# Kernel optimization log

Measured on AMD Instinct MI355X. Metric: run time of the kernel, lower is better.

## Reference

```python
import jax, jax.numpy as jnp
import numpy as np

# Model hyperparameters (from init_kwargs)
SIG = 10.0      # kernel length scale 'sig'
C = 0.0         # energy integration constant 'c'
STD = 1.0       # data std 'std'
N_ATOMS = 21    # aspirin-like molecule
T_ROWS = 12000  # n_train * n_perms (permutation-expanded training rows)
DESC = N_ATOMS * (N_ATOMS - 1) // 2  # 210
BATCH = 64


def setup_inputs() -> dict:
    key = jax.random.key(0)
    k1, k2, k3 = jax.random.split(key, 3)
    # Geometries: M x N x 3 Cartesian coordinates (spread out so atoms are distinct)
    Rs = jax.random.normal(k1, (BATCH, N_ATOMS, 3), dtype=jnp.float32) * 2.0
    # Permutation-expanded training descriptors (inverse distances -> positive)
    xs_train = jax.random.uniform(k2, (T_ROWS, DESC), dtype=jnp.float32, minval=0.05, maxval=1.0)
    Jx_alphas = jax.random.normal(k3, (T_ROWS, DESC), dtype=jnp.float32)
    return {"Rs": Rs, "xs_train": xs_train, "Jx_alphas": Jx_alphas}


def reference(Rs, xs_train, Jx_alphas):
    sig = SIG
    q = np.sqrt(5.0) / sig
    M, N, _ = Rs.shape
    i, j = np.tril_indices(N, k=-1)

    # Pairwise atomic displacement vectors and distances. Diagonal is padded with 1
    # (instead of inf as in the torch code) -- every diagonal contribution below is
    # multiplied by an exact zero (expand_tril zeroes the diagonal, diffs diag = 0),
    # so the value is irrelevant but this keeps gradients finite.
    diffs = Rs[:, :, None, :] - Rs[:, None, :, :]          # [M, N, N, 3]
    eye = jnp.eye(N, dtype=Rs.dtype)
    dists = jnp.sqrt(jnp.sum(diffs * diffs, axis=-1) + eye)  # [M, N, N]

    # Inverse-distance descriptor (strict lower triangle)
    xs = 1.0 / dists[:, i, j]                              # [M, DESC]

    # Descriptor-space differences vs all (permuted) training points
    x_diffs = (q * xs)[:, None, :] - q * xs_train[None]    # [M, T, DESC]
    x_dists = jnp.sqrt(jnp.sum(x_diffs * x_diffs, axis=-1))  # [M, T]

    # Matern-5/2 kernel pieces
    exp_xs = (5.0 / (3.0 * sig * sig)) * jnp.exp(-x_dists)   # [M, T]
    dot_x_diff_Jx = jnp.einsum('mtd,td->mt', x_diffs, Jx_alphas)  # [M, T]
    exp_xs_1_x_dists = exp_xs * (1.0 + x_dists)              # [M, T]

    # Descriptor-space force pieces
    F1s_x = jnp.einsum('mt,mtd->md', exp_xs * dot_x_diff_Jx, x_diffs)  # [M, DESC]
    F2s_x = exp_xs_1_x_dists @ Jx_alphas                               # [M, DESC]
    Fs_x = (F1s_x - F2s_x) * STD

    # expand_tril: scatter descriptor-space forces into symmetric NxN with zero diag
    full = jnp.zeros((M, N, N), dtype=Rs.dtype)
    full = full.at[:, i, j].set(Fs_x).at[:, j, i].set(Fs_x)

    # Cartesian forces: sum over first atom index (torch's .sum(dim=1))
    Fs = jnp.einsum('mab,mabk->mbk', full / dists ** 3, diffs)  # [M, N, 3]

    # Energies
    Es = jnp.sum(exp_xs_1_x_dists * dot_x_diff_Jx, axis=-1) / q
    Es = C + Es * STD
    return Es, Fs
```

## Files before the change

kernel.cpp:

```cpp
#include <hip/hip_runtime.h>
#include <hip/hip_fp16.h>
#include <math.h>

#define N_ATOMS 21
#define DESC 210
#define APAD 224
#define T_ROWS 12000
#define BATCH 64
#define NBLK_A 250
#define TROWS_B 48
#define PCW 216

#define QCONST 0.22360679774997896f
#define K0CONST (1.0f/60.0f)

typedef short bf16x8 __attribute__((ext_vector_type(8)));
typedef float f32x4 __attribute__((ext_vector_type(4)));

__device__ __forceinline__ float u2f(unsigned int u) {
    union { unsigned int u; float f; } x; x.u = u; return x.f;
}
__device__ __forceinline__ unsigned short f2bf(float f) {
    union { float f; unsigned int u; } x; x.f = f;
    unsigned int r = x.u + 0x7fffu + ((x.u >> 16) & 1u);
    return (unsigned short)(r >> 16);
}
__device__ __forceinline__ float bf2f(unsigned short h) {
    return u2f((unsigned int)h << 16);
}

__global__ __launch_bounds__(256) void k_prep(const float* __restrict__ Rs,
                                              unsigned short* __restrict__ Abf,
                                              float* __restrict__ na2) {
    int m = blockIdx.x;
    __shared__ float R[N_ATOMS * 3];
    __shared__ float red[256];
    int tid = threadIdx.x;
    if (tid < N_ATOMS * 3) R[tid] = Rs[m * N_ATOMS * 3 + tid];
    __syncthreads();
    float val = 0.f;
    if (tid < DESC) {
        int p = tid;
        int i = (int)((1.0f + sqrtf(1.0f + 8.0f * (float)p)) * 0.5f);
        while (i * (i - 1) / 2 > p) --i;
        while ((i + 1) * i / 2 <= p) ++i;
        int j = p - i * (i - 1) / 2;
        float dx = R[i * 3 + 0] - R[j * 3 + 0];
        float dy = R[i * 3 + 1] - R[j * 3 + 1];
        float dz = R[i * 3 + 2] - R[j * 3 + 2];
        float d = sqrtf(dx * dx + dy * dy + dz * dz);
        val = QCONST / d;
    }
    unsigned short h = f2bf(val);
    if (tid < APAD) Abf[m * APAD + tid] = h;
    float va = bf2f(h);
    red[tid] = va * va;
    __syncthreads();
    for (int s = 128; s > 0; s >>= 1) {
        if (tid < s) red[tid] += red[tid + s];
        __syncthreads();
    }
    if (tid == 0) na2[m] = red[0];
}

#define BS_OFF 0
#define JS_OFF 22272
#define XT_OFF 44544
#define W_OFF  91136
#define NB_OFF 104448
#define BJ_OFF 104640
#define NA_OFF 104832
#define LDS_SZ 105088

__global__ __launch_bounds__(256) void k_fused(const float* __restrict__ Btr,
                                               const float* __restrict__ Jx,
                                               const unsigned short* __restrict__ Abf,
                                               const float* __restrict__ na2,
                                               float* __restrict__ es_p,
                                               float* __restrict__ rs_p,
                                               __half* __restrict__ pC) {
    __shared__ char lds[LDS_SZ];
    const int blk = blockIdx.x;
    const int t0 = blk * TROWS_B;
    const int tid = threadIdx.x;
    const int lane = tid & 63;
    const int w = __builtin_amdgcn_readfirstlane(tid >> 6);
    const int lr = lane & 15;
    const int kb = lane >> 4;

    uint4 au[7];
    {
        const unsigned short* ap = Abf + (w * 16 + lr) * APAD + kb * 8;
#pragma unroll
        for (int k8 = 0; k8 < 7; k8++) au[k8] = *(const uint4*)(ap + k8 * 32);
    }
    if (tid < 64) *(float*)(lds + NA_OFF + tid * 4) = na2[tid];

#pragma unroll
    for (int pass = 0; pass < 2; ++pass) {
        if (pass == 1 && tid >= 128) break;
        const int g = pass * 32 + (tid >> 3);
        const int gl = tid & 7;
        const int tr = t0 + g;
        const float* bp = Btr + (size_t)tr * DESC;
        const float* jp = Jx + (size_t)tr * DESC;
        float nb = 0.f, bj = 0.f;
#pragma unroll
        for (int it = 0; it < 15; it++) {
            int c = it * 8 + gl;
            if (c < 116) {
                float2 vb = make_float2(0.f, 0.f), vj = make_float2(0.f, 0.f);
                if (c < 105) {
                    vb = *(const float2*)(bp + 2 * c);
                    vj = *(const float2*)(jp + 2 * c);
                }
                unsigned short hbx = f2bf(vb.x), hby = f2bf(vb.y);
                unsigned short hjx = f2bf(vj.x), hjy = f2bf(vj.y);
                *(unsigned int*)(lds + BS_OFF + g * 464 + c * 4) = (unsigned)hbx | ((unsigned)hby << 16);
                *(unsigned int*)(lds + JS_OFF + g * 464 + c * 4) = (unsigned)hjx | ((unsigned)hjy << 16);
                if (c < 112) {
                    const int d = 2 * c;
                    *(unsigned short*)(lds + XT_OFF + d * 208 + g * 2) = hbx;
                    *(unsigned short*)(lds + XT_OFF + (d + 1) * 208 + g * 2) = hby;
                    *(unsigned short*)(lds + XT_OFF + d * 208 + 96 + g * 2) = hjx;
                    *(unsigned short*)(lds + XT_OFF + (d + 1) * 208 + 96 + g * 2) = hjy;
                }
                float fbx = bf2f(hbx), fby = bf2f(hby);
                float fjx = bf2f(hjx), fjy = bf2f(hjy);
                nb = fmaf(fbx, fbx, nb); nb = fmaf(fby, fby, nb);
                bj = fmaf(fbx, fjx, bj); bj = fmaf(fby, fjy, bj);
            }
        }
#pragma unroll
        for (int m = 1; m < 8; m <<= 1) { nb += __shfl_xor(nb, m); bj += __shfl_xor(bj, m); }
        if (gl == 0) {
            *(float*)(lds + NB_OFF + g * 4) = nb;
            *(float*)(lds + BJ_OFF + g * 4) = bj;
        }
    }
    __syncthreads();

    f32x4 accP[3] = {{0.f,0.f,0.f,0.f},{0.f,0.f,0.f,0.f},{0.f,0.f,0.f,0.f}};
    f32x4 accQ[3] = {{0.f,0.f,0.f,0.f},{0.f,0.f,0.f,0.f},{0.f,0.f,0.f,0.f}};
#pragma unroll
    for (int k8 = 0; k8 < 7; k8++) {
        union { uint4 u; bf16x8 h; } a;
        a.u = au[k8];
#pragma unroll
        for (int nt = 0; nt < 3; nt++) {
            union { uint4 u; bf16x8 h; } bu, ju;
            const int ro = (nt * 16 + lr) * 464 + k8 * 64 + kb * 16;
            bu.u = *(const uint4*)(lds + BS_OFF + ro);
            ju.u = *(const uint4*)(lds + JS_OFF + ro);
            accP[nt] = __builtin_amdgcn_mfma_f32_16x16x32_bf16(a.h, bu.h, accP[nt], 0, 0, 0);
            accQ[nt] = __builtin_amdgcn_mfma_f32_16x16x32_bf16(a.h, ju.h, accQ[nt], 0, 0, 0);
        }
    }

    float na4[4];
#pragma unroll
    for (int r = 0; r < 4; r++)
        na4[r] = *(const float*)(lds + NA_OFF + (w * 16 + kb * 4 + r) * 4);
    float es4[4] = {0.f,0.f,0.f,0.f}, rs4[4] = {0.f,0.f,0.f,0.f};
#pragma unroll
    for (int nt = 0; nt < 3; nt++) {
        const int row = nt * 16 + lr;
        const float nb_c = *(const float*)(lds + NB_OFF + row * 4);
        const float bj_c = *(const float*)(lds + BJ_OFF + row * 4);
#pragma unroll
        for (int r = 0; r < 4; r++) {
            float S = na4[r] + QCONST * QCONST * nb_c - 2.f * QCONST * accP[nt][r];
            float xd = sqrtf(fmaxf(S, 0.f));
            float e = K0CONST * __expf(-xd);
            float dot = accQ[nt][r] - QCONST * bj_c;
            float w1 = e * dot;
            float w2 = e * (1.f + xd);
            es4[r] += w2 * dot; rs4[r] += w1;
            const int mrow = w * 16 + kb * 4 + r;
            *(unsigned short*)(lds + W_OFF + mrow * 208 + row * 2) = f2bf(QCONST * w1);
            *(unsigned short*)(lds + W_OFF + mrow * 208 + 96 + row * 2) = f2bf(w2);
        }
    }
#pragma unroll
    for (int m = 1; m < 16; m <<= 1) {
#pragma unroll
        for (int r = 0; r < 4; r++) {
            es4[r] += __shfl_xor(es4[r], m);
            rs4[r] += __shfl_xor(rs4[r], m);
        }
    }
    if (lr == 0) {
#pragma unroll
        for (int r = 0; r < 4; r++) {
            es_p[(size_t)(w * 16 + kb * 4 + r) * NBLK_A + blk] = es4[r];
            rs_p[(size_t)(w * 16 + kb * 4 + r) * NBLK_A + blk] = rs4[r];
        }
    }
    __syncthreads();

    {
        union { uint4 u; bf16x8 h; } wa[3];
        const char* Wp = lds + W_OFF + (w * 16 + lr) * 208;
#pragma unroll
        for (int c = 0; c < 3; c++) wa[c].u = *(const uint4*)(Wp + c * 64 + kb * 16);
        __half* D = (__half*)lds;
#pragma unroll
        for (int dt = 0; dt < 14; dt++) {
            const char* Xp = lds + XT_OFF + (dt * 16 + lr) * 208;
            f32x4 acc = {0.f, 0.f, 0.f, 0.f};
#pragma unroll
            for (int c = 0; c < 3; c++) {
                union { uint4 u; bf16x8 h; } xb;
                xb.u = *(const uint4*)(Xp + c * 64 + kb * 16);
                acc = __builtin_amdgcn_mfma_f32_16x16x32_bf16(wa[c].h, xb.h, acc, 0, 0, 0);
            }
#pragma unroll
            for (int r = 0; r < 4; r++)
                D[(w * 16 + kb * 4 + r) * 224 + dt * 16 + lr] = __float2half(acc[r]);
        }
    }
    __syncthreads();

    {
        const char* D = (const char*)lds;
        for (int i = tid; i < 64 * 27; i += 256) {
            const int mrow = i / 27, oct = i % 27;
            uint4 v = *(const uint4*)(D + mrow * 448 + oct * 16);
            *(uint4*)((char*)pC + (((size_t)mrow * NBLK_A + blk) * PCW + oct * 8) * 2) = v;
        }
    }
}

__global__ __launch_bounds__(256) void k_final(const float* __restrict__ Rs,
                                               const unsigned short* __restrict__ Abf,
                                               const float* __restrict__ es_p,
                                               const float* __restrict__ rs_p,
                                               const __half* __restrict__ pC,
                                               float* __restrict__ out) {
    const int m = blockIdx.x;
    const int tid = threadIdx.x;
    __shared__ float parts[27][8][8];
    __shared__ float fsx[DESC];
    __shared__ float R[N_ATOMS * 3];
    __shared__ float s_rs, s_es;
    if (tid < N_ATOMS * 3) R[tid] = Rs[m * N_ATOMS * 3 + tid];
    if (tid < 216) {
        const int cg = tid / 27, o = tid % 27;
        float facc[8];
#pragma unroll
        for (int e = 0; e < 8; e++) facc[e] = 0.f;
        const __half* base = pC + (size_t)m * NBLK_A * PCW + o * 8;
#pragma unroll 4
        for (int c = cg; c < NBLK_A; c += 8) {
            uint4 v = *(const uint4*)(base + (size_t)c * PCW);
            const __half2* h = (const __half2*)&v;
#pragma unroll
            for (int p2 = 0; p2 < 4; p2++) {
                float2 f = __half22float2(h[p2]);
                facc[p2 * 2] += f.x;
                facc[p2 * 2 + 1] += f.y;
            }
        }
#pragma unroll
        for (int e = 0; e < 8; e++) parts[o][cg][e] = facc[e];
    }
    __syncthreads();
    if (tid < 64) {
        float es = 0.f, rs = 0.f;
        for (int c2 = tid; c2 < NBLK_A; c2 += 64) {
            es += es_p[(size_t)m * NBLK_A + c2];
            rs += rs_p[(size_t)m * NBLK_A + c2];
        }
        for (int mask = 1; mask < 64; mask <<= 1) {
            es += __shfl_xor(es, mask);
            rs += __shfl_xor(rs, mask);
        }
        if (tid == 0) { s_es = es; s_rs = rs; }
    }
    __syncthreads();
    if (tid < DESC) {
        float s = 0.f;
        const int o = tid >> 3, e = tid & 7;
#pragma unroll
        for (int cg = 0; cg < 8; cg++) s += parts[o][cg][e];
        fsx[tid] = s_rs * bf2f(Abf[m * APAD + tid]) - s;
    }
    if (tid == 0) out[m] = s_es * (1.0f / QCONST);
    __syncthreads();
    if (tid < N_ATOMS * 3) {
        int b = tid / 3, kk = tid % 3;
        float acc = 0.f;
        for (int a = 0; a < N_ATOMS; a++) {
            if (a == b) continue;
            float dx = R[a * 3 + 0] - R[b * 3 + 0];
            float dy = R[a * 3 + 1] - R[b * 3 + 1];
            float dz = R[a * 3 + 2] - R[b * 3 + 2];
            float d2 = dx * dx + dy * dy + dz * dz;
            float dist = sqrtf(d2);
            float inv3 = 1.0f / (d2 * dist);
            int hi = (a > b) ? a : b, lo = (a > b) ? b : a;
            int p = hi * (hi - 1) / 2 + lo;
            float diffk = (kk == 0) ? dx : ((kk == 1) ? dy : dz);
            acc = fmaf(fsx[p] * inv3, diffk, acc);
        }
        out[BATCH + m * N_ATOMS * 3 + tid] = acc;
    }
}

extern "C" void kernel_launch(void* const* d_in, const int* in_sizes, int n_in,
                              void* d_out, int out_size, void* d_ws, size_t ws_size,
                              hipStream_t stream) {
    (void)in_sizes; (void)n_in; (void)out_size; (void)ws_size;
    const float* Rs = (const float*)d_in[0];
    const float* Btr = (const float*)d_in[1];
    const float* Jx = (const float*)d_in[2];
    float* out = (float*)d_out;

    char* ws = (char*)d_ws;
    unsigned short* Abf = (unsigned short*)ws;  ws += (size_t)BATCH * APAD * 2;
    float* na2 = (float*)ws;                    ws += BATCH * 4;
    float* es_p = (float*)ws;                   ws += (size_t)BATCH * NBLK_A * 4;
    float* rs_p = (float*)ws;                   ws += (size_t)BATCH * NBLK_A * 4;
    __half* pC = (__half*)ws;

    k_prep<<<dim3(BATCH), dim3(256), 0, stream>>>(Rs, Abf, na2);
    k_fused<<<dim3(NBLK_A), dim3(256), 0, stream>>>(Btr, Jx, Abf, na2, es_p, rs_p, pC);
    k_final<<<dim3(BATCH), dim3(256), 0, stream>>>(Rs, Abf, es_p, rs_p, pC, out);
}
```

Before: 33.32 us.

## Fold descriptor prep into fused kernel and widen blocks to 512 threads

Removes the separate prep kernel: every fused block recomputes all 64 inverse-distance descriptors and their norms into LDS, and block 0 writes them out for the final kernel. The fused and final kernels move to 512 threads, splitting the MFMA tiles and the load work across twice as many waves, with per-block partial energy sums reduced in LDS first. This saves one launch and raises occupancy and latency hiding, at the cost of redundant descriptor work in every block and extra barriers.

Result: slower. 39.90 us (+19.8%).

```diff
diff --git a/kernel.cpp b/kernel.cpp
--- a/kernel.cpp
+++ b/kernel.cpp
@@ -7,7 +7,7 @@
 #define APAD 224
 #define T_ROWS 12000
 #define BATCH 64
-#define NBLK_A 250
+#define NBLK 250
 #define TROWS_B 48
 #define PCW 216
 
@@ -27,40 +27,6 @@
 }
 __device__ __forceinline__ float bf2f(unsigned short h) {
     return u2f((unsigned int)h << 16);
-}
-
-__global__ __launch_bounds__(256) void k_prep(const float* __restrict__ Rs,
-                                              unsigned short* __restrict__ Abf,
-                                              float* __restrict__ na2) {
-    int m = blockIdx.x;
-    __shared__ float R[N_ATOMS * 3];
-    __shared__ float red[256];
-    int tid = threadIdx.x;
-    if (tid < N_ATOMS * 3) R[tid] = Rs[m * N_ATOMS * 3 + tid];
-    __syncthreads();
-    float val = 0.f;
-    if (tid < DESC) {
-        int p = tid;
-        int i = (int)((1.0f + sqrtf(1.0f + 8.0f * (float)p)) * 0.5f);
-        while (i * (i - 1) / 2 > p) --i;
-        while ((i + 1) * i / 2 <= p) ++i;
-        int j = p - i * (i - 1) / 2;
-        float dx = R[i * 3 + 0] - R[j * 3 + 0];
-        float dy = R[i * 3 + 1] - R[j * 3 + 1];
-        float dz = R[i * 3 + 2] - R[j * 3 + 2];
-        float d = sqrtf(dx * dx + dy * dy + dz * dz);
-        val = QCONST / d;
-    }
-    unsigned short h = f2bf(val);
-    if (tid < APAD) Abf[m * APAD + tid] = h;
-    float va = bf2f(h);
-    red[tid] = va * va;
-    __syncthreads();
-    for (int s = 128; s > 0; s >>= 1) {
-        if (tid < s) red[tid] += red[tid + s];
-        __syncthreads();
-    }
-    if (tid == 0) na2[m] = red[0];
 }
 
 #define BS_OFF 0
@@ -70,12 +36,13 @@
 #define NB_OFF 104448
 #define BJ_OFF 104640
 #define NA_OFF 104832
-#define LDS_SZ 105088
-
-__global__ __launch_bounds__(256) void k_fused(const float* __restrict__ Btr,
+#define ES_OFF 105088
+#define LDS_SZ 106624
+
+__global__ __launch_bounds__(512) void k_fused(const float* __restrict__ Rs,
+                                               const float* __restrict__ Btr,
                                                const float* __restrict__ Jx,
-                                               const unsigned short* __restrict__ Abf,
-                                               const float* __restrict__ na2,
+                                               unsigned short* __restrict__ Abf,
                                                float* __restrict__ es_p,
                                                float* __restrict__ rs_p,
                                                __half* __restrict__ pC) {
@@ -87,125 +54,203 @@
     const int w = __builtin_amdgcn_readfirstlane(tid >> 6);
     const int lr = lane & 15;
     const int kb = lane >> 4;
-
+    const int mt = w & 3;
+    const int half = w >> 2;
+
+    {
+        float* rl = (float*)(lds + JS_OFF);
+        for (int i = tid; i < BATCH * 63; i += 512) rl[i] = Rs[i];
+    }
+    __syncthreads();
+    {
+        const float* rl = (const float*)(lds + JS_OFF);
+        for (int i = tid; i < BATCH * APAD; i += 512) {
+            const int m = i / APAD, p = i - m * APAD;
+            unsigned short h = 0;
+            if (p < DESC) {
+                int ia = (int)((1.0f + sqrtf(1.0f + 8.0f * (float)p)) * 0.5f);
+                while (ia * (ia - 1) / 2 > p) --ia;
+                while ((ia + 1) * ia / 2 <= p) ++ia;
+                int ja = p - ia * (ia - 1) / 2;
+                const float* Rm = rl + m * 63;
+                float dx = Rm[ia * 3 + 0] - Rm[ja * 3 + 0];
+                float dy = Rm[ia * 3 + 1] - Rm[ja * 3 + 1];
+                float dz = Rm[ia * 3 + 2] - Rm[ja * 3 + 2];
+                h = f2bf(QCONST / sqrtf(dx * dx + dy * dy + dz * dz));
+            }
+            *(unsigned short*)(lds + XT_OFF + m * 448 + p * 2) = h;
+        }
+    }
+    __syncthreads();
     uint4 au[7];
     {
-        const unsigned short* ap = Abf + (w * 16 + lr) * APAD + kb * 8;
-#pragma unroll
-        for (int k8 = 0; k8 < 7; k8++) au[k8] = *(const uint4*)(ap + k8 * 32);
-    }
-    if (tid < 64) *(float*)(lds + NA_OFF + tid * 4) = na2[tid];
+        const char* ap = lds + XT_OFF + (mt * 16 + lr) * 448 + kb * 16;
+#pragma unroll
+        for (int k8 = 0; k8 < 7; k8++) au[k8] = *(const uint4*)(ap + k8 * 64);
+    }
+    {
+        const int m = tid >> 3, gl = tid & 7;
+        float s = 0.f;
+#pragma unroll
+        for (int it = 0; it < 4; it++) {
+            const int c16 = it * 8 + gl;
+            if (c16 < 28) {
+                uint4 v = *(const uint4*)(lds + XT_OFF + m * 448 + c16 * 16);
+                const unsigned int* vv = (const unsigned int*)&v;
+#pragma unroll
+                for (int q2 = 0; q2 < 4; q2++) {
+                    float lo = u2f(vv[q2] << 16), hi = u2f(vv[q2] & 0xFFFF0000u);
+                    s = fmaf(lo, lo, s); s = fmaf(hi, hi, s);
+                }
+            }
+        }
+#pragma unroll
+        for (int msk = 1; msk < 8; msk <<= 1) s += __shfl_xor(s, msk);
+        if (gl == 0) *(float*)(lds + NA_OFF + m * 4) = s;
+    }
+    if (blk == 0) {
+        for (int i = tid; i < BATCH * 28; i += 512) {
+            uint4 v = *(const uint4*)(lds + XT_OFF + i * 16);
+            *(uint4*)((char*)Abf + i * 16) = v;
+        }
+    }
+    __syncthreads();
 
 #pragma unroll
     for (int pass = 0; pass < 2; ++pass) {
-        if (pass == 1 && tid >= 128) break;
-        const int g = pass * 32 + (tid >> 3);
-        const int gl = tid & 7;
-        const int tr = t0 + g;
-        const float* bp = Btr + (size_t)tr * DESC;
-        const float* jp = Jx + (size_t)tr * DESC;
-        float nb = 0.f, bj = 0.f;
+        if (pass == 1 && tid >= 256) break;
+        const int g = tid >> 3, gl = tid & 7;
+        int arr, row;
+        if (pass == 0) { arr = (g >= 48) ? 1 : 0; row = arr ? (g - 48) : g; }
+        else           { arr = 1; row = 16 + g; }
+        const float* sp = (arr ? Jx : Btr) + (size_t)(t0 + row) * DESC;
+        char* const rdst = lds + (arr ? JS_OFF : BS_OFF) + row * 464;
+        const int xtc = arr ? (96 + row * 2) : (row * 2);
 #pragma unroll
         for (int it = 0; it < 15; it++) {
-            int c = it * 8 + gl;
+            const int c = it * 8 + gl;
             if (c < 116) {
-                float2 vb = make_float2(0.f, 0.f), vj = make_float2(0.f, 0.f);
-                if (c < 105) {
-                    vb = *(const float2*)(bp + 2 * c);
-                    vj = *(const float2*)(jp + 2 * c);
-                }
-                unsigned short hbx = f2bf(vb.x), hby = f2bf(vb.y);
-                unsigned short hjx = f2bf(vj.x), hjy = f2bf(vj.y);
-                *(unsigned int*)(lds + BS_OFF + g * 464 + c * 4) = (unsigned)hbx | ((unsigned)hby << 16);
-                *(unsigned int*)(lds + JS_OFF + g * 464 + c * 4) = (unsigned)hjx | ((unsigned)hjy << 16);
+                float2 v = make_float2(0.f, 0.f);
+                if (c < 105) v = *(const float2*)(sp + 2 * c);
+                unsigned short hx = f2bf(v.x), hy = f2bf(v.y);
+                *(unsigned int*)(rdst + c * 4) = (unsigned)hx | ((unsigned)hy << 16);
                 if (c < 112) {
                     const int d = 2 * c;
-                    *(unsigned short*)(lds + XT_OFF + d * 208 + g * 2) = hbx;
-                    *(unsigned short*)(lds + XT_OFF + (d + 1) * 208 + g * 2) = hby;
-                    *(unsigned short*)(lds + XT_OFF + d * 208 + 96 + g * 2) = hjx;
-                    *(unsigned short*)(lds + XT_OFF + (d + 1) * 208 + 96 + g * 2) = hjy;
+                    *(unsigned short*)(lds + XT_OFF + d * 208 + xtc) = hx;
+                    *(unsigned short*)(lds + XT_OFF + (d + 1) * 208 + xtc) = hy;
                 }
-                float fbx = bf2f(hbx), fby = bf2f(hby);
-                float fjx = bf2f(hjx), fjy = bf2f(hjy);
-                nb = fmaf(fbx, fbx, nb); nb = fmaf(fby, fby, nb);
-                bj = fmaf(fbx, fjx, bj); bj = fmaf(fby, fjy, bj);
-            }
-        }
-#pragma unroll
-        for (int m = 1; m < 8; m <<= 1) { nb += __shfl_xor(nb, m); bj += __shfl_xor(bj, m); }
+            }
+        }
+    }
+    __syncthreads();
+
+    if (tid < 384) {
+        const int row = tid >> 3, gl = tid & 7;
+        float nb = 0.f, bj = 0.f;
+#pragma unroll
+        for (int it = 0; it < 15; it++) {
+            const int c = it * 8 + gl;
+            if (c < 105) {
+                unsigned int ub = *(const unsigned int*)(lds + BS_OFF + row * 464 + c * 4);
+                unsigned int uj = *(const unsigned int*)(lds + JS_OFF + row * 464 + c * 4);
+                float bx = u2f(ub << 16), by = u2f(ub & 0xFFFF0000u);
+                float jx2 = u2f(uj << 16), jy2 = u2f(uj & 0xFFFF0000u);
+                nb = fmaf(bx, bx, nb); nb = fmaf(by, by, nb);
+                bj = fmaf(bx, jx2, bj); bj = fmaf(by, jy2, bj);
+            }
+        }
+#pragma unroll
+        for (int msk = 1; msk < 8; msk <<= 1) { nb += __shfl_xor(nb, msk); bj += __shfl_xor(bj, msk); }
         if (gl == 0) {
-            *(float*)(lds + NB_OFF + g * 4) = nb;
-            *(float*)(lds + BJ_OFF + g * 4) = bj;
-        }
-    }
-    __syncthreads();
-
-    f32x4 accP[3] = {{0.f,0.f,0.f,0.f},{0.f,0.f,0.f,0.f},{0.f,0.f,0.f,0.f}};
-    f32x4 accQ[3] = {{0.f,0.f,0.f,0.f},{0.f,0.f,0.f,0.f},{0.f,0.f,0.f,0.f}};
+            *(float*)(lds + NB_OFF + row * 4) = nb;
+            *(float*)(lds + BJ_OFF + row * 4) = bj;
+        }
+    }
+
+    const int nt0 = (half == 0) ? 0 : 1;
+    const int nnt = (half == 0) ? 1 : 2;
+    f32x4 accP[2] = {{0.f,0.f,0.f,0.f},{0.f,0.f,0.f,0.f}};
+    f32x4 accQ[2] = {{0.f,0.f,0.f,0.f},{0.f,0.f,0.f,0.f}};
 #pragma unroll
     for (int k8 = 0; k8 < 7; k8++) {
         union { uint4 u; bf16x8 h; } a;
         a.u = au[k8];
 #pragma unroll
-        for (int nt = 0; nt < 3; nt++) {
-            union { uint4 u; bf16x8 h; } bu, ju;
-            const int ro = (nt * 16 + lr) * 464 + k8 * 64 + kb * 16;
-            bu.u = *(const uint4*)(lds + BS_OFF + ro);
-            ju.u = *(const uint4*)(lds + JS_OFF + ro);
-            accP[nt] = __builtin_amdgcn_mfma_f32_16x16x32_bf16(a.h, bu.h, accP[nt], 0, 0, 0);
-            accQ[nt] = __builtin_amdgcn_mfma_f32_16x16x32_bf16(a.h, ju.h, accQ[nt], 0, 0, 0);
-        }
-    }
+        for (int s = 0; s < 2; s++) {
+            if (s < nnt) {
+                const int nt = nt0 + s;
+                union { uint4 u; bf16x8 h; } bu, ju;
+                const int ro = (nt * 16 + lr) * 464 + k8 * 64 + kb * 16;
+                bu.u = *(const uint4*)(lds + BS_OFF + ro);
+                ju.u = *(const uint4*)(lds + JS_OFF + ro);
+                accP[s] = __builtin_amdgcn_mfma_f32_16x16x32_bf16(a.h, bu.h, accP[s], 0, 0, 0);
+                accQ[s] = __builtin_amdgcn_mfma_f32_16x16x32_bf16(a.h, ju.h, accQ[s], 0, 0, 0);
+            }
+        }
+    }
+    __syncthreads();
 
     float na4[4];
 #pragma unroll
     for (int r = 0; r < 4; r++)
-        na4[r] = *(const float*)(lds + NA_OFF + (w * 16 + kb * 4 + r) * 4);
-    float es4[4] = {0.f,0.f,0.f,0.f}, rs4[4] = {0.f,0.f,0.f,0.f};
-#pragma unroll
-    for (int nt = 0; nt < 3; nt++) {
-        const int row = nt * 16 + lr;
-        const float nb_c = *(const float*)(lds + NB_OFF + row * 4);
-        const float bj_c = *(const float*)(lds + BJ_OFF + row * 4);
-#pragma unroll
-        for (int r = 0; r < 4; r++) {
-            float S = na4[r] + QCONST * QCONST * nb_c - 2.f * QCONST * accP[nt][r];
-            float xd = sqrtf(fmaxf(S, 0.f));
-            float e = K0CONST * __expf(-xd);
-            float dot = accQ[nt][r] - QCONST * bj_c;
-            float w1 = e * dot;
-            float w2 = e * (1.f + xd);
-            es4[r] += w2 * dot; rs4[r] += w1;
-            const int mrow = w * 16 + kb * 4 + r;
-            *(unsigned short*)(lds + W_OFF + mrow * 208 + row * 2) = f2bf(QCONST * w1);
-            *(unsigned short*)(lds + W_OFF + mrow * 208 + 96 + row * 2) = f2bf(w2);
-        }
-    }
-#pragma unroll
-    for (int m = 1; m < 16; m <<= 1) {
-#pragma unroll
-        for (int r = 0; r < 4; r++) {
-            es4[r] += __shfl_xor(es4[r], m);
-            rs4[r] += __shfl_xor(rs4[r], m);
-        }
-    }
-    if (lr == 0) {
-#pragma unroll
-        for (int r = 0; r < 4; r++) {
-            es_p[(size_t)(w * 16 + kb * 4 + r) * NBLK_A + blk] = es4[r];
-            rs_p[(size_t)(w * 16 + kb * 4 + r) * NBLK_A + blk] = rs4[r];
-        }
-    }
-    __syncthreads();
+        na4[r] = *(const float*)(lds + NA_OFF + (mt * 16 + kb * 4 + r) * 4);
+#pragma unroll
+    for (int s = 0; s < 2; s++) {
+        if (s < nnt) {
+            const int nt = nt0 + s;
+            const int row = nt * 16 + lr;
+            const float nb_c = *(const float*)(lds + NB_OFF + row * 4);
+            const float bj_c = *(const float*)(lds + BJ_OFF + row * 4);
+            float es4[4], rs4[4];
+#pragma unroll
+            for (int r = 0; r < 4; r++) {
+                float S = na4[r] + QCONST * QCONST * nb_c - 2.f * QCONST * accP[s][r];
+                float xd = sqrtf(fmaxf(S, 0.f));
+                float e = K0CONST * __expf(-xd);
+                float dot = accQ[s][r] - QCONST * bj_c;
+                float w1 = e * dot;
+                float w2 = e * (1.f + xd);
+                es4[r] = w2 * dot; rs4[r] = w1;
+                const int mrow = mt * 16 + kb * 4 + r;
+                *(unsigned short*)(lds + W_OFF + mrow * 208 + row * 2) = f2bf(QCONST * w1);
+                *(unsigned short*)(lds + W_OFF + mrow * 208 + 96 + row * 2) = f2bf(w2);
+            }
+#pragma unroll
+            for (int msk = 1; msk < 16; msk <<= 1) {
+#pragma unroll
+                for (int r = 0; r < 4; r++) {
+                    es4[r] += __shfl_xor(es4[r], msk);
+                    rs4[r] += __shfl_xor(rs4[r], msk);
+                }
+            }
+            if (lr == 0) {
+#pragma unroll
+                for (int r = 0; r < 4; r++) {
+                    const int m = mt * 16 + kb * 4 + r;
+                    *(float*)(lds + ES_OFF + (nt * 64 + m) * 4) = es4[r];
+                    *(float*)(lds + ES_OFF + 768 + (nt * 64 + m) * 4) = rs4[r];
+                }
+            }
+        }
+    }
+    __syncthreads();
+
+    if (tid < 64) {
+        const float* esl = (const float*)(lds + ES_OFF);
+        const float* rsl = (const float*)(lds + ES_OFF + 768);
+        es_p[(size_t)tid * NBLK + blk] = esl[tid] + esl[64 + tid] + esl[128 + tid];
+        rs_p[(size_t)tid * NBLK + blk] = rsl[tid] + rsl[64 + tid] + rsl[128 + tid];
+    }
 
     {
         union { uint4 u; bf16x8 h; } wa[3];
-        const char* Wp = lds + W_OFF + (w * 16 + lr) * 208;
+        const char* Wp = lds + W_OFF + (mt * 16 + lr) * 208;
 #pragma unroll
         for (int c = 0; c < 3; c++) wa[c].u = *(const uint4*)(Wp + c * 64 + kb * 16);
         __half* D = (__half*)lds;
 #pragma unroll
-        for (int dt = 0; dt < 14; dt++) {
+        for (int j = 0; j < 7; j++) {
+            const int dt = half * 7 + j;
             const char* Xp = lds + XT_OFF + (dt * 16 + lr) * 208;
             f32x4 acc = {0.f, 0.f, 0.f, 0.f};
 #pragma unroll
@@ -216,22 +261,22 @@
             }
 #pragma unroll
             for (int r = 0; r < 4; r++)
-                D[(w * 16 + kb * 4 + r) * 224 + dt * 16 + lr] = __float2half(acc[r]);
+                D[(mt * 16 + kb * 4 + r) * 224 + dt * 16 + lr] = __float2half(acc[r]);
         }
     }
     __syncthreads();
 
     {
         const char* D = (const char*)lds;
-        for (int i = tid; i < 64 * 27; i += 256) {
+        for (int i = tid; i < 64 * 27; i += 512) {
             const int mrow = i / 27, oct = i % 27;
             uint4 v = *(const uint4*)(D + mrow * 448 + oct * 16);
-            *(uint4*)((char*)pC + (((size_t)mrow * NBLK_A + blk) * PCW + oct * 8) * 2) = v;
-        }
-    }
-}
-
-__global__ __launch_bounds__(256) void k_final(const float* __restrict__ Rs,
+            *(uint4*)((char*)pC + (((size_t)mrow * NBLK + blk) * PCW + oct * 8) * 2) = v;
+        }
+    }
+}
+
+__global__ __launch_bounds__(512) void k_final(const float* __restrict__ Rs,
                                                const unsigned short* __restrict__ Abf,
                                                const float* __restrict__ es_p,
                                                const float* __restrict__ rs_p,
@@ -239,19 +284,18 @@
                                                float* __restrict__ out) {
     const int m = blockIdx.x;
     const int tid = threadIdx.x;
-    __shared__ float parts[27][8][8];
+    __shared__ float parts[27][16][8];
     __shared__ float fsx[DESC];
     __shared__ float R[N_ATOMS * 3];
     __shared__ float s_rs, s_es;
     if (tid < N_ATOMS * 3) R[tid] = Rs[m * N_ATOMS * 3 + tid];
-    if (tid < 216) {
+    if (tid < 432) {
         const int cg = tid / 27, o = tid % 27;
         float facc[8];
 #pragma unroll
         for (int e = 0; e < 8; e++) facc[e] = 0.f;
-        const __half* base = pC + (size_t)m * NBLK_A * PCW + o * 8;
-#pragma unroll 4
-        for (int c = cg; c < NBLK_A; c += 8) {
+        const __half* base = pC + (size_t)m * NBLK * PCW + o * 8;
+        for (int c = cg; c < NBLK; c += 16) {
             uint4 v = *(const uint4*)(base + (size_t)c * PCW);
             const __half2* h = (const __half2*)&v;
 #pragma unroll
@@ -263,32 +307,31 @@
         }
 #pragma unroll
         for (int e = 0; e < 8; e++) parts[o][cg][e] = facc[e];
-    }
-    __syncthreads();
-    if (tid < 64) {
+    } else if (tid >= 448) {
+        const int lx = tid - 448;
         float es = 0.f, rs = 0.f;
-        for (int c2 = tid; c2 < NBLK_A; c2 += 64) {
-            es += es_p[(size_t)m * NBLK_A + c2];
-            rs += rs_p[(size_t)m * NBLK_A + c2];
-        }
-        for (int mask = 1; mask < 64; mask <<= 1) {
-            es += __shfl_xor(es, mask);
-            rs += __shfl_xor(rs, mask);
-        }
-        if (tid == 0) { s_es = es; s_rs = rs; }
+        for (int c2 = lx; c2 < NBLK; c2 += 64) {
+            es += es_p[(size_t)m * NBLK + c2];
+            rs += rs_p[(size_t)m * NBLK + c2];
+        }
+        for (int msk = 1; msk < 64; msk <<= 1) {
+            es += __shfl_xor(es, msk);
+            rs += __shfl_xor(rs, msk);
+        }
+        if (lx == 0) { s_es = es; s_rs = rs; }
     }
     __syncthreads();
     if (tid < DESC) {
         float s = 0.f;
         const int o = tid >> 3, e = tid & 7;
 #pragma unroll
-        for (int cg = 0; cg < 8; cg++) s += parts[o][cg][e];
+        for (int cg = 0; cg < 16; cg++) s += parts[o][cg][e];
         fsx[tid] = s_rs * bf2f(Abf[m * APAD + tid]) - s;
     }
     if (tid == 0) out[m] = s_es * (1.0f / QCONST);
     __syncthreads();
     if (tid < N_ATOMS * 3) {
-        int b = tid / 3, kk = tid % 3;
+        const int b = tid / 3, kk = tid % 3;
         float acc = 0.f;
         for (int a = 0; a < N_ATOMS; a++) {
             if (a == b) continue;
@@ -318,12 +361,10 @@
 
     char* ws = (char*)d_ws;
     unsigned short* Abf = (unsigned short*)ws;  ws += (size_t)BATCH * APAD * 2;
-    float* na2 = (float*)ws;                    ws += BATCH * 4;
-    float* es_p = (float*)ws;                   ws += (size_t)BATCH * NBLK_A * 4;
-    float* rs_p = (float*)ws;                   ws += (size_t)BATCH * NBLK_A * 4;
+    float* es_p = (float*)ws;                   ws += (size_t)BATCH * NBLK * 4;
+    float* rs_p = (float*)ws;                   ws += (size_t)BATCH * NBLK * 4;
     __half* pC = (__half*)ws;
 
-    k_prep<<<dim3(BATCH), dim3(256), 0, stream>>>(Rs, Abf, na2);
-    k_fused<<<dim3(NBLK_A), dim3(256), 0, stream>>>(Btr, Jx, Abf, na2, es_p, rs_p, pC);
-    k_final<<<dim3(BATCH), dim3(256), 0, stream>>>(Rs, Abf, es_p, rs_p, pC, out);
-}
+    k_fused<<<dim3(NBLK), dim3(512), 0, stream>>>(Rs, Btr, Jx, Abf, es_p, rs_p, pC);
+    k_final<<<dim3(BATCH), dim3(512), 0, stream>>>(Rs, Abf, es_p, rs_p, pC, out);
+}
```
